# Kernel optimization log

Hardware: AMD Instinct MI355X
Metric: run time of the kernel (lower is better)

The kernel has to match this reference:

```python
import jax, jax.numpy as jnp
import numpy as np

B, L, P = 65536, 512, 96
E_LIN, E = 14, 16
FFT = 512
TEMP = 0.07
K = 2
EPS = 1e-5


def setup_inputs() -> dict:
    key = jax.random.key(0)
    k0, k1, k2 = jax.random.split(key, 3)
    x = jax.random.normal(k0, (B, L), dtype=jnp.float32)
    Wg = jax.random.normal(k1, (E, FFT // 2), dtype=jnp.float32) * 0.02
    bg = jnp.zeros((E,), dtype=jnp.float32)
    Wr = jax.random.normal(k2, (E_LIN, P, L), dtype=jnp.float32) * 0.02
    br = jnp.zeros((E_LIN, P), dtype=jnp.float32)
    return {"x": x, "Wg": Wg, "bg": bg, "Wr": Wr, "br": br}


def _periodogram(x):
    # x: [B, L] -> normalized power spectrum [B, FFT//2]
    x0 = x - jnp.mean(x, axis=1, keepdims=True)
    dft = jnp.fft.fft(x0, n=FFT, axis=1) / np.float32(np.sqrt(FFT))
    dft = dft[:, : FFT // 2]
    I = dft.real ** 2 + dft.imag ** 2
    s = jnp.sum(I, axis=1, keepdims=True)
    s = jnp.where(s == 0, jnp.ones_like(s), s)
    return I / s


def reference(x, Wg, bg, Wr, br):
    # gating (eval mode: no noise, divide by temperature)
    I = _periodogram(x)                                  # [B, F/2]
    gate = (I @ Wg.T + bg) / TEMP                        # [B, E]
    topv, topi = jax.lax.top_k(gate, K)                  # [B, K]
    gates = jax.nn.softmax(topv, axis=1)                 # [B, K]

    # RLinear experts: RevIN(norm) -> Linear -> RevIN(denorm); stats detached
    mu = jax.lax.stop_gradient(jnp.mean(x, axis=1, keepdims=True))        # [B,1]
    sd = jax.lax.stop_gradient(jnp.sqrt(jnp.var(x, axis=1, keepdims=True) + EPS))
    xn = (x - mu) / sd                                   # [B, L]
    yr = jnp.einsum('bl,epl->bep', xn, Wr) + br          # [B, E_LIN, P]
    yr = yr * sd[:, :, None] + mu[:, :, None]

    mean_out = jnp.broadcast_to(jnp.mean(x, axis=1, keepdims=True), (x.shape[0], P))[:, None, :]
    naive_out = jnp.broadcast_to(x[:, -1:], (x.shape[0], P))[:, None, :]

    eo = jnp.concatenate([yr, mean_out, naive_out], axis=1)   # [B, E, P]
    sel = jnp.take_along_axis(eo, topi[:, :, None], axis=1)   # [B, K, P]
    out = jnp.sum(gates[:, :, None] * sel, axis=1)            # [B, P]
    return out
```

## Files before the change

kernel.cpp:

```cpp
#include <hip/hip_runtime.h>
#include <math.h>

#define NB_B 65536
#define NL   512
#define NP   96
#define NE   16
#define NEL  14
#define NF   256
#define TEMP_INV (1.0f/0.07f)
#define TAU  1e-5f
#define PI_D 3.14159265358979323846
#define MAXCHK 1280

typedef __attribute__((ext_vector_type(8))) short bf16x8;
typedef __attribute__((ext_vector_type(4))) float f32x4;


#define WS_PCNT     0
#define WS_PTK      16384
#define WS_PBASE    32768
#define WS_FLAGCNT  33792
#define WS_NCHK     33824
#define WS_FLAG     33856
#define WS_SSUM     296000
#define WS_WGT      301376
#define WS_BGT      317760
#define WS_TWF      317824
#define WS_TWD      319872
#define WS_REC      328064
#define WS_HDR      590208
#define WS_RIDX     1638784
#define WS_WRB      1900928
#define WS_DESC     3473792
#define WS_XB16     3480064

__device__ __forceinline__ unsigned short f2bf(float f) {
    unsigned u = __float_as_uint(f);
    unsigned r = (u + 0x7fffu + ((u >> 16) & 1u)) >> 16;
    return (unsigned short)r;
}

__global__ __launch_bounds__(256) void k_prep(
    const float* __restrict__ Wg, const float* __restrict__ bg,
    const float* __restrict__ Wr,
    float* __restrict__ Ssum, float* __restrict__ WgE, float* __restrict__ bgT,
    float2* __restrict__ twf, double2* __restrict__ twd,
    int* __restrict__ pcnt, int* __restrict__ flagcnt,
    ushort4* __restrict__ Wrb)
{
    int g = blockIdx.x * 256 + threadIdx.x;
    {
        ushort4 o = make_ushort4(0, 0, 0, 0);
        if (g < NEL * NP * NL / 4) {
            float4 v = ((const float4*)Wr)[g];
            o.x = f2bf(v.x); o.y = f2bf(v.y); o.z = f2bf(v.z); o.w = f2bf(v.w);
        }
        Wrb[g] = o;
    }
    if (g < NEL * NP) {
        const float4* w = (const float4*)(Wr + (size_t)g * NL);
        float s = 0.f;
        for (int i = 0; i < NL / 4; i++) { float4 v = w[i]; s += v.x + v.y + v.z + v.w; }
        Ssum[g] = s;
    }
    if (g < 4096) {
        int c = g & 3, e = (g >> 2) & 15, f4 = g >> 6;
        WgE[g] = Wg[e * NF + f4 * 4 + c] * TEMP_INV;
    }
    if (g < NF) {
        double a = -2.0 * PI_D * (double)g / 512.0;
        twf[g] = make_float2((float)cos(a), (float)sin(a));
    }
    if (g < 512) {
        double a = -2.0 * PI_D * (double)g / 512.0;
        twd[g] = make_double2(cos(a), sin(a));
    }
    if (g < 256) pcnt[g << 4] = 0;
    if (g < NE) bgT[g] = bg[g] * TEMP_INV;
    if (g == 300) *flagcnt = 0;
}

__global__ __launch_bounds__(256) void k_gate(
    const float* __restrict__ x,
    const float4* __restrict__ WgE4, const float* __restrict__ bgT,
    const float2* __restrict__ twf,
    int* __restrict__ rec, float4* __restrict__ hdr,
    int* __restrict__ flaglist, int* __restrict__ flagcnt,
    int* __restrict__ pcnt, unsigned short* __restrict__ xb16)
{
    __shared__ float2 s_tw[256];
    __shared__ __align__(16) float2 s_z[4][576];
    float* s_Iv = (float*)&s_z[0][0];

    const int t = threadIdx.x;
    const int wv = t >> 6, l = t & 63;
    const int b0 = blockIdx.x * 8 + wv * 2;
    s_tw[t] = twf[t];

    const float2 w2 = twf[l << 2];
    float2 wst[5];
    wst[0] = twf[(l & 31) << 3];
    wst[1] = twf[(l & 15) << 4];
    wst[2] = twf[(l & 7) << 5];
    wst[3] = twf[(l & 3) << 6];
    wst[4] = twf[(l & 1) << 7];

    const float* xa = x + (size_t)b0 * NL;
    const float* xb = xa + NL;
    float xr[8], xi[8];
#pragma unroll
    for (int k = 0; k < 8; k++) { xr[k] = xa[k * 64 + l]; xi[k] = xb[k * 64 + l]; }
    const float last_a = __shfl(xr[7], 63);
    const float last_b = __shfl(xi[7], 63);

    if (xb16) {
        unsigned short* pa = xb16 + (size_t)b0 * NL + l;
        unsigned short* pb = pa + NL;
#pragma unroll
        for (int k = 0; k < 8; k++) {
            pa[k * 64] = f2bf(xr[k]);
            pb[k * 64] = f2bf(xi[k]);
        }
    }
    __syncthreads();

#pragma unroll
    for (int k = 0; k < 4; k++) {
        float2 w = s_tw[k * 64 + l];
        float ur = xr[k], ui = xi[k], vr = xr[k + 4], vi = xi[k + 4];
        xr[k] = ur + vr; xi[k] = ui + vi;
        float dr = ur - vr, di = ui - vi;
        xr[k + 4] = dr * w.x - di * w.y; xi[k + 4] = dr * w.y + di * w.x;
    }
    {
        const int kk[4] = {0, 1, 4, 5};
#pragma unroll
        for (int g2 = 0; g2 < 4; g2++) {
            int k = kk[g2];
            float2 w = s_tw[((k & 1) * 64 + l) << 1];
            float ur = xr[k], ui = xi[k], vr = xr[k + 2], vi = xi[k + 2];
            xr[k] = ur + vr; xi[k] = ui + vi;
            float dr = ur - vr, di = ui - vi;
            xr[k + 2] = dr * w.x - di * w.y; xi[k + 2] = dr * w.y + di * w.x;
        }
    }
    {
#pragma unroll
        for (int k = 0; k < 8; k += 2) {
            float ur = xr[k], ui = xi[k], vr = xr[k + 1], vi = xi[k + 1];
            xr[k] = ur + vr; xi[k] = ui + vi;
            float dr = ur - vr, di = ui - vi;
            xr[k + 1] = dr * w2.x - di * w2.y; xi[k + 1] = dr * w2.y + di * w2.x;
        }
    }
#pragma unroll
    for (int st = 3; st < 8; st++) {
        const int half = 256 >> st;
        const float2 w = wst[st - 3];
        const bool up = (l & half) != 0;
        const float sg = up ? -1.f : 1.f;
        const float cc = up ? w.x : 1.f;
        const float ss = up ? w.y : 0.f;
#pragma unroll
        for (int k = 0; k < 8; k++) {
            float pr = __shfl_xor(xr[k], half);
            float pi = __shfl_xor(xi[k], half);
            float tr = fmaf(sg, xr[k], pr);
            float ti = fmaf(sg, xi[k], pi);
            xr[k] = tr * cc - ti * ss;
            xi[k] = tr * ss + ti * cc;
        }
    }
    {
        const float sg = (l & 1) ? -1.f : 1.f;
#pragma unroll
        for (int k = 0; k < 8; k++) {
            float pr = __shfl_xor(xr[k], 1);
            float pi = __shfl_xor(xi[k], 1);
            xr[k] = fmaf(sg, xr[k], pr);
            xi[k] = fmaf(sg, xi[k], pi);
        }
    }

#pragma unroll
    for (int k = 0; k < 8; k++) {
        int i = k * 64 + l;
        s_z[wv][i + (i >> 3)] = make_float2(xr[k], xi[k]);
    }

    float Ia[4], Ib[4];
    float psa = 0.f, psb = 0.f;
#pragma unroll
    for (int j = 0; j < 4; j++) {
        int f = (l << 2) | j;
        int i1_ = (int)(__brev((unsigned)f) >> 23);
        int i2_ = (int)(__brev((unsigned)((512 - f) & 511)) >> 23);
        float2 z1 = s_z[wv][i1_ + (i1_ >> 3)];
        float2 z2 = s_z[wv][i2_ + (i2_ >> 3)];
        float pr_ = z1.x + z2.x, qm = z1.y - z2.y;
        float qp = z1.y + z2.y, pm = z1.x - z2.x;
        float va = pr_ * pr_ + qm * qm;
        float vb = qp * qp + pm * pm;
        if (f == 0) { va = 0.f; vb = 0.f; }
        Ia[j] = va; Ib[j] = vb;
        psa += va; psb += vb;
    }
#pragma unroll
    for (int m = 1; m < 64; m <<= 1) {
        psa += __shfl_xor(psa, m); psb += __shfl_xor(psb, m);
    }
    const float psa_raw = psa, psb_raw = psb;
    if (psa == 0.f) psa = 1.f;
    if (psb == 0.f) psb = 1.f;
    const float inv_a = 1.f / psa, inv_b = 1.f / psb;

    const float2 Z0   = s_z[wv][0];
    const float2 Z256 = s_z[wv][1];

    float* wI = s_Iv + wv * 1152;
    const int io = (l << 2) + ((l >> 4) << 2);
    *(float4*)(wI + io)       = make_float4(Ia[0], Ia[1], Ia[2], Ia[3]);
    *(float4*)(wI + 272 + io) = make_float4(Ib[0], Ib[1], Ib[2], Ib[3]);

    const int e16 = l & 15, cq = l >> 4;
    const float bgv = bgT[e16];
    float accA = 0.f, accB = 0.f;
    const float* rA = wI + cq * 68;
    const float* rB = rA + 272;
#pragma unroll 4
    for (int jj = 0; jj < 16; jj++) {
        float4 ia = *(const float4*)(rA + 4 * jj);
        float4 ib = *(const float4*)(rB + 4 * jj);
        float4 w = WgE4[(cq * 16 + jj) * 16 + e16];
        accA += ia.x * w.x + ia.y * w.y + ia.z * w.z + ia.w * w.w;
        accB += ib.x * w.x + ib.y * w.y + ib.z * w.z + ib.w * w.w;
    }
    accA += __shfl_xor(accA, 16); accA += __shfl_xor(accA, 32);
    accB += __shfl_xor(accB, 16); accB += __shfl_xor(accB, 32);

    float v = ((l & 16) ? accB * inv_b : accA * inv_a) + bgv;

    float b0v = v; int b0i = e16;
#pragma unroll
    for (int m = 1; m < 16; m <<= 1) {
        float ov = __shfl_xor(b0v, m); int oi = __shfl_xor(b0i, m);
        if (ov > b0v || (ov == b0v && oi < b0i)) { b0v = ov; b0i = oi; }
    }
    float v1 = (e16 == b0i) ? -1e30f : v;
    float b1v = v1; int b1i = e16;
#pragma unroll
    for (int m = 1; m < 16; m <<= 1) {
        float ov = __shfl_xor(b1v, m); int oi = __shfl_xor(b1i, m);
        if (ov > b1v || (ov == b1v && oi < b1i)) { b1v = ov; b1i = oi; }
    }
    float v2 = (e16 == b1i) ? -1e30f : v1;
    float b2v = v2;
#pragma unroll
    for (int m = 1; m < 16; m <<= 1) {
        float ov = __shfl_xor(b2v, m);
        b2v = fmaxf(b2v, ov);
    }

    if (l == 0 || l == 16) {
        const int r = l >> 4;
        const int b = b0 + r;
        const float mu = (r ? Z0.y : Z0.x) * (1.f / 512.f);
        const float Jv = r ? Z256.y : Z256.x;
        const float ps = r ? psb_raw : psa_raw;
        const float sd = sqrtf((0.5f * ps + Jv * Jv) * (1.f / 262144.f) + 1e-5f);
        const float last = r ? last_b : last_a;
        const float w0 = 1.f / (1.f + expf(b1v - b0v));
        const int pid = b0i * 16 + b1i;
        rec[b] = pid;
        hdr[b] = make_float4(mu, sd, last, w0);
        atomicAdd(&pcnt[pid << 4], 1);
        if (b1v - b2v < TAU) {
            int pos = atomicAdd(flagcnt, 1);
            flaglist[pos] = b;
        }
    }
}

__global__ __launch_bounds__(256) void k_refine(
    const float* __restrict__ x, const double2* __restrict__ twd,
    const float* __restrict__ Wg, const float* __restrict__ bg,
    int* __restrict__ rec, float4* __restrict__ hdr,
    const int* __restrict__ flaglist, const int* __restrict__ flagcnt,
    int* __restrict__ pcnt)
{
    __shared__ double s_x[512];
    __shared__ double s_I[256];
    __shared__ double s_red[16];
    __shared__ double s_g[16];
    const int nf = *flagcnt;
    const int t = threadIdx.x;
    const int wid = t >> 6, lane = t & 63;
    for (int fi = blockIdx.x; fi < nf; fi += gridDim.x) {
        const int b = flaglist[fi];
        const float* xp = x + (size_t)b * NL;
        double v0 = (double)xp[t], v1 = (double)xp[t + 256];
        double lsum = v0 + v1;
        for (int m = 1; m < 64; m <<= 1) lsum += __shfl_xor(lsum, m);
        if (lane == 0) s_red[wid] = lsum;
        __syncthreads();
        double mu = (s_red[0] + s_red[1] + s_red[2] + s_red[3]) * (1.0 / 512.0);
        s_x[t] = v0 - mu; s_x[t + 256] = v1 - mu;
        __syncthreads();
        double2 w = twd[t];
        double pr = 1.0, pi = 0.0, cr = 0.0, ci = 0.0;
        for (int n = 0; n < 512; n++) {
            double xv = s_x[n];
            cr += xv * pr; ci += xv * pi;
            double t2 = pr * w.x - pi * w.y;
            pi = pr * w.y + pi * w.x;
            pr = t2;
        }
        double I = cr * cr + ci * ci;
        s_I[t] = I;
        double ls = I;
        for (int m = 1; m < 64; m <<= 1) ls += __shfl_xor(ls, m);
        if (lane == 0) s_red[8 + wid] = ls;
        __syncthreads();
        double stot = s_red[8] + s_red[9] + s_red[10] + s_red[11];
        if (stot == 0.0) stot = 1.0;
        if (t < 16) {
            double acc = 0.0;
            const float* wrow = Wg + t * NF;
            for (int f = 0; f < NF; f++) acc += s_I[f] * (double)wrow[f];
            s_g[t] = (acc / stot + (double)bg[t]) * (1.0 / 0.07);
        }
        __syncthreads();
        if (t == 0) {
            double c0 = -1e300, c1 = -1e300; int j0 = 0, j1 = 0;
            for (int i = 0; i < 16; i++) {
                double v = s_g[i];
                if (v > c0) { c1 = c0; j1 = j0; c0 = v; j0 = i; }
                else if (v > c1) { c1 = v; j1 = i; }
            }
            double e1 = exp(c1 - c0);
            float w0f = (float)(1.0 / (1.0 + e1));
            int newpid = j0 * 16 + j1;
            int old = rec[b];
            if (newpid != old) {
                atomicSub(&pcnt[old << 4], 1);
                atomicAdd(&pcnt[newpid << 4], 1);
                rec[b] = newpid;
            }
            ((float*)(hdr + b))[3] = w0f;
        }
        __syncthreads();
    }
}

__global__ __launch_bounds__(256) void k_scan(
    const int* __restrict__ pcnt, int* __restrict__ pbase, int* __restrict__ ptk,
    int* __restrict__ desc, int* __restrict__ nchk)
{
    __shared__ int s[256], c[256];
    const int t = threadIdx.x;
    const int n = pcnt[t << 4];
    s[t] = n;
    c[t] = (n + 63) >> 6;
    __syncthreads();
    for (int off = 1; off < 256; off <<= 1) {
        int v1 = (t >= off) ? s[t - off] : 0;
        int v2 = (t >= off) ? c[t - off] : 0;
        __syncthreads();
        s[t] += v1; c[t] += v2;
        __syncthreads();
    }
    int excl = t ? s[t - 1] : 0;
    int cexcl = t ? c[t - 1] : 0;
    pbase[t] = excl;
    ptk[t << 4] = excl;
    int myc = (n + 63) >> 6;
    for (int j = 0; j < myc; j++) desc[cexcl + j] = (t << 16) | j;
    if (t == 255) *nchk = cexcl + myc;
}

__global__ __launch_bounds__(256) void k_scatter(
    const int* __restrict__ rec, int* __restrict__ ptk, int* __restrict__ ridx)
{
    __shared__ int h[256], base_[256];
    const int t = threadIdx.x;
    const int b = blockIdx.x * 256 + t;
    h[t] = 0;
    __syncthreads();
    int pid = rec[b];
    int lo = atomicAdd(&h[pid], 1);
    __syncthreads();
    if (h[t]) base_[t] = atomicAdd(&ptk[t << 4], h[t]);
    __syncthreads();
    ridx[base_[pid] + lo] = b;
}

template<int XB>
__global__ __launch_bounds__(256) void k_gemm(
    const float* __restrict__ x, const unsigned short* __restrict__ xb16,
    const unsigned short* __restrict__ Wrb,
    const float* __restrict__ br, const float* __restrict__ Ssum,
    const float4* __restrict__ hdr, float* __restrict__ out,
    const int* __restrict__ pcnt, const int* __restrict__ pbase,
    const int* __restrict__ ridx,
    const int* __restrict__ desc, const int* __restrict__ nchk)
{
    __shared__ __align__(16) unsigned short sA[64 * 72];
    __shared__ __align__(16) unsigned short sB[2][96 * 72];
    __shared__ int    s_idx[64];
    __shared__ float4 s_hdr[64];
    __shared__ float  s_br[2][96], s_S[2][96];
    if ((int)blockIdx.x >= *nchk) return;
    const int d = desc[blockIdx.x];
    const int pid = d >> 16, cc = d & 0xffff;
    const int n = pcnt[pid << 4];
    const int base = pbase[pid];
    const int i0 = pid >> 4, i1 = pid & 15;
    const int t = threadIdx.x;
    const int lane = t & 63, wv = t >> 6;
    const int quad = lane >> 4, l16 = lane & 15;
    const int ar = t >> 2, asub = t & 3;
    if (t < 96) {
        s_br[0][t] = (i0 < NEL) ? br[i0 * NP + t] : 0.f;
        s_S [0][t] = (i0 < NEL) ? Ssum[i0 * NP + t] : 0.f;
        s_br[1][t] = (i1 < NEL) ? br[i1 * NP + t] : 0.f;
        s_S [1][t] = (i1 < NEL) ? Ssum[i1 * NP + t] : 0.f;
    }
    if (t < 64) {
        int g = cc * 64 + t;
        bool vld = g < n;
        int row = vld ? ridx[base + g] : -1;
        s_idx[t] = row;
        s_hdr[t] = vld ? hdr[row] : make_float4(0.f, 0.f, 0.f, 0.f);
    }
    __syncthreads();

    f32x4 acc[2][6];
#pragma unroll
    for (int ex = 0; ex < 2; ex++)
#pragma unroll
        for (int j = 0; j < 6; j++) acc[ex][j] = (f32x4){0.f, 0.f, 0.f, 0.f};

    int rr = s_idx[ar]; if (rr < 0) rr = s_idx[0];

    unsigned boff[6];
    unsigned short* bdst[6];
    const unsigned short* wb[2];
    wb[0] = Wrb + (size_t)i0 * NP * NL;
    wb[1] = Wrb + (size_t)i1 * NP * NL;
    int bex[6];
#pragma unroll
    for (int it = 0; it < 6; it++) {
        int ex = (it >= 3);
        int fl = t + (it - 3 * ex) * 256;
        int p = fl >> 3, kg = fl & 7;
        bex[it] = ex;
        boff[it] = (unsigned)(p * NL + kg * 8);
        bdst[it] = &sB[ex][p * 72 + kg * 8];
    }
    unsigned short* adst = sA + ar * 72 + asub * 16;

    const unsigned short* xrow16 = xb16 + (size_t)rr * NL + asub * 16;
    const float* xrowf = x + (size_t)rr * NL + asub * 16;

    bf16x8 aR[2]; float4 fA[4]; bf16x8 bR[6];

    if constexpr (XB) {
        aR[0] = *(const bf16x8*)(xrow16);
        aR[1] = *(const bf16x8*)(xrow16 + 8);
    } else {
#pragma unroll
        for (int i = 0; i < 4; i++) fA[i] = ((const float4*)xrowf)[i];
    }
#pragma unroll
    for (int it = 0; it < 6; it++) bR[it] = *(const bf16x8*)(wb[bex[it]] + boff[it]);

    for (int kb = 0; kb < NL; kb += 64) {
        if constexpr (XB) {
            *(bf16x8*)adst       = aR[0];
            *(bf16x8*)(adst + 8) = aR[1];
        } else {
            unsigned short tmp[16];
#pragma unroll
            for (int i = 0; i < 4; i++) {
                float4 v = fA[i];
                tmp[i * 4 + 0] = f2bf(v.x); tmp[i * 4 + 1] = f2bf(v.y);
                tmp[i * 4 + 2] = f2bf(v.z); tmp[i * 4 + 3] = f2bf(v.w);
            }
            *(bf16x8*)adst       = *(bf16x8*)tmp;
            *(bf16x8*)(adst + 8) = *(bf16x8*)(tmp + 8);
        }
#pragma unroll
        for (int it = 0; it < 6; it++) *(bf16x8*)bdst[it] = bR[it];
        __syncthreads();

        const int kn = kb + 64;
        if (kn < NL) {
            if constexpr (XB) {
                aR[0] = *(const bf16x8*)(xrow16 + kn);
                aR[1] = *(const bf16x8*)(xrow16 + kn + 8);
            } else {
#pragma unroll
                for (int i = 0; i < 4; i++) fA[i] = ((const float4*)(xrowf + kn))[i];
            }
#pragma unroll
            for (int it = 0; it < 6; it++)
                bR[it] = *(const bf16x8*)(wb[bex[it]] + boff[it] + kn);
        }

#pragma unroll
        for (int ks = 0; ks < 2; ks++) {
            bf16x8 af = *(const bf16x8*)(sA + (wv * 16 + l16) * 72 + ks * 32 + quad * 8);
#pragma unroll
            for (int ex = 0; ex < 2; ex++)
#pragma unroll
                for (int nt = 0; nt < 6; nt++) {
                    bf16x8 bf = *(const bf16x8*)(&sB[ex][(nt * 16 + l16) * 72 + ks * 32 + quad * 8]);
                    acc[ex][nt] = __builtin_amdgcn_mfma_f32_16x16x32_bf16(af, bf, acc[ex][nt], 0, 0, 0);
                }
        }
        __syncthreads();
    }
#pragma unroll
    for (int i = 0; i < 4; i++) {
        int rloc = wv * 16 + quad * 4 + i;
        int row = s_idx[rloc];
        if (row >= 0) {
            float4 h = s_hdr[rloc];
            float mu = h.x, sd = h.y, last = h.z, w0 = h.w, w1 = 1.f - w0;
            float* orow = out + (size_t)row * NP;
#pragma unroll
            for (int nt = 0; nt < 6; nt++) {
                int p = nt * 16 + l16;
                float v0 = (i0 < NEL) ? (mu + s_br[0][p] * sd - mu * s_S[0][p] + acc[0][nt][i])
                                      : (i0 == NEL ? mu : last);
                float v1 = (i1 < NEL) ? (mu + s_br[1][p] * sd - mu * s_S[1][p] + acc[1][nt][i])
                                      : (i1 == NEL ? mu : last);
                orow[p] = w0 * v0 + w1 * v1;
            }
        }
    }
}

extern "C" void kernel_launch(void* const* d_in, const int* in_sizes, int n_in,
                              void* d_out, int out_size, void* d_ws, size_t ws_size,
                              hipStream_t stream)
{
    const float* x  = (const float*)d_in[0];
    const float* Wg = (const float*)d_in[1];
    const float* bg = (const float*)d_in[2];
    const float* Wr = (const float*)d_in[3];
    const float* br = (const float*)d_in[4];
    float* out = (float*)d_out;
    char* ws = (char*)d_ws;

    int*     pcnt     = (int*)(ws + WS_PCNT);
    int*     ptk      = (int*)(ws + WS_PTK);
    int*     pbase    = (int*)(ws + WS_PBASE);
    int*     flagcnt  = (int*)(ws + WS_FLAGCNT);
    int*     nchk     = (int*)(ws + WS_NCHK);
    int*     flaglist = (int*)(ws + WS_FLAG);
    float*   Ssum     = (float*)(ws + WS_SSUM);
    float*   WgE      = (float*)(ws + WS_WGT);
    float*   bgT      = (float*)(ws + WS_BGT);
    float2*  twf      = (float2*)(ws + WS_TWF);
    double2* twd      = (double2*)(ws + WS_TWD);
    int*     rec      = (int*)(ws + WS_REC);
    float4*  hdr      = (float4*)(ws + WS_HDR);
    int*     ridx     = (int*)(ws + WS_RIDX);
    unsigned short* Wrb = (unsigned short*)(ws + WS_WRB);
    int*     desc     = (int*)(ws + WS_DESC);

    const size_t xb_bytes = (size_t)NB_B * NL * 2;
    const int use_xb = (ws_size >= (size_t)WS_XB16 + xb_bytes);
    unsigned short* xb16 = use_xb ? (unsigned short*)(ws + WS_XB16) : (unsigned short*)0;

    k_prep<<<dim3(768), dim3(256), 0, stream>>>(Wg, bg, Wr, Ssum, WgE, bgT, twf, twd,
                                                pcnt, flagcnt, (ushort4*)Wrb);
    k_gate<<<dim3(NB_B / 8), dim3(256), 0, stream>>>(x, (const float4*)WgE, bgT, twf,
                                                     rec, hdr, flaglist, flagcnt, pcnt, xb16);
    k_refine<<<dim3(512), dim3(256), 0, stream>>>(x, twd, Wg, bg, rec, hdr,
                                                  flaglist, flagcnt, pcnt);
    k_scan<<<dim3(1), dim3(256), 0, stream>>>(pcnt, pbase, ptk, desc, nchk);
    k_scatter<<<dim3(NB_B / 256), dim3(256), 0, stream>>>(rec, ptk, ridx);
    if (use_xb)
        k_gemm<1><<<dim3(MAXCHK), dim3(256), 0, stream>>>(x, xb16, Wrb, br, Ssum, hdr, out,
                                                          pcnt, pbase, ridx, desc, nchk);
    else
        k_gemm<0><<<dim3(MAXCHK), dim3(256), 0, stream>>>(x, xb16, Wrb, br, Ssum, hdr, out,
                                                          pcnt, pbase, ridx, desc, nchk);
}
```

Baseline: 319.9 us.

## Permute bf16 x and Wr layouts for vectorized stores; keep twiddles in registers

The gating kernel now writes each lane's eight bf16 x values as one 16-byte vector store instead of eight strided 2-byte stores. This makes the xb16 layout a permutation of the sequence dimension, and the prep kernel applies the same permutation to the bf16 expert weights so the GEMM dot products are unchanged. Twiddle factors for the first two FFT stages are loaded into registers, which removes the shared-memory staging and a block barrier. The prep kernel's strided gathers from Wr cost more there, but that kernel is small.

After: 320.9 us. No clear change (+0.3%).

```diff
diff --git a/kernel.cpp b/kernel.cpp
--- a/kernel.cpp
+++ b/kernel.cpp
@@ -46,13 +46,22 @@
     float* __restrict__ Ssum, float* __restrict__ WgE, float* __restrict__ bgT,
     float2* __restrict__ twf, double2* __restrict__ twd,
     int* __restrict__ pcnt, int* __restrict__ flagcnt,
-    ushort4* __restrict__ Wrb)
+    ushort4* __restrict__ Wrb, int perm)
 {
     int g = blockIdx.x * 256 + threadIdx.x;
     {
         ushort4 o = make_ushort4(0, 0, 0, 0);
         if (g < NEL * NP * NL / 4) {
-            float4 v = ((const float4*)Wr)[g];
+            float4 v;
+            if (perm) {
+                int row = g >> 7, sq = g & 127;
+                int ll = sq >> 1, kb = (sq & 1) * 4;
+                const float* wr = Wr + (size_t)row * NL + ll;
+                v.x = wr[(kb + 0) * 64]; v.y = wr[(kb + 1) * 64];
+                v.z = wr[(kb + 2) * 64]; v.w = wr[(kb + 3) * 64];
+            } else {
+                v = ((const float4*)Wr)[g];
+            }
             o.x = f2bf(v.x); o.y = f2bf(v.y); o.z = f2bf(v.z); o.w = f2bf(v.w);
         }
         Wrb[g] = o;
@@ -88,15 +97,18 @@
     int* __restrict__ flaglist, int* __restrict__ flagcnt,
     int* __restrict__ pcnt, unsigned short* __restrict__ xb16)
 {
-    __shared__ float2 s_tw[256];
     __shared__ __align__(16) float2 s_z[4][576];
     float* s_Iv = (float*)&s_z[0][0];
 
     const int t = threadIdx.x;
     const int wv = t >> 6, l = t & 63;
     const int b0 = blockIdx.x * 8 + wv * 2;
-    s_tw[t] = twf[t];
-
+
+    float2 tw0[4], tw1[2];
+#pragma unroll
+    for (int k = 0; k < 4; k++) tw0[k] = twf[k * 64 + l];
+    tw1[0] = twf[2 * l];
+    tw1[1] = twf[128 + 2 * l];
     const float2 w2 = twf[l << 2];
     float2 wst[5];
     wst[0] = twf[(l & 31) << 3];
@@ -114,19 +126,16 @@
     const float last_b = __shfl(xi[7], 63);
 
     if (xb16) {
-        unsigned short* pa = xb16 + (size_t)b0 * NL + l;
-        unsigned short* pb = pa + NL;
-#pragma unroll
-        for (int k = 0; k < 8; k++) {
-            pa[k * 64] = f2bf(xr[k]);
-            pb[k * 64] = f2bf(xi[k]);
-        }
-    }
-    __syncthreads();
+        unsigned short ta[8], tb[8];
+#pragma unroll
+        for (int k = 0; k < 8; k++) { ta[k] = f2bf(xr[k]); tb[k] = f2bf(xi[k]); }
+        *(bf16x8*)(xb16 + (size_t)b0 * NL + l * 8)       = *(bf16x8*)ta;
+        *(bf16x8*)(xb16 + (size_t)(b0 + 1) * NL + l * 8) = *(bf16x8*)tb;
+    }
 
 #pragma unroll
     for (int k = 0; k < 4; k++) {
-        float2 w = s_tw[k * 64 + l];
+        float2 w = tw0[k];
         float ur = xr[k], ui = xi[k], vr = xr[k + 4], vi = xi[k + 4];
         xr[k] = ur + vr; xi[k] = ui + vi;
         float dr = ur - vr, di = ui - vi;
@@ -137,7 +146,7 @@
 #pragma unroll
         for (int g2 = 0; g2 < 4; g2++) {
             int k = kk[g2];
-            float2 w = s_tw[((k & 1) * 64 + l) << 1];
+            float2 w = tw1[k & 1];
             float ur = xr[k], ui = xi[k], vr = xr[k + 2], vi = xi[k + 2];
             xr[k] = ur + vr; xi[k] = ui + vi;
             float dr = ur - vr, di = ui - vi;
@@ -575,7 +584,7 @@
     unsigned short* xb16 = use_xb ? (unsigned short*)(ws + WS_XB16) : (unsigned short*)0;
 
     k_prep<<<dim3(768), dim3(256), 0, stream>>>(Wg, bg, Wr, Ssum, WgE, bgT, twf, twd,
-                                                pcnt, flagcnt, (ushort4*)Wrb);
+                                                pcnt, flagcnt, (ushort4*)Wrb, use_xb);
     k_gate<<<dim3(NB_B / 8), dim3(256), 0, stream>>>(x, (const float4*)WgE, bgT, twf,
                                                      rec, hdr, flaglist, flagcnt, pcnt, xb16);
     k_refine<<<dim3(512), dim3(256), 0, stream>>>(x, twd, Wg, bg, rec, hdr,
```
